# Kernel optimization log

Measured on AMD Instinct MI355X. Metric: run time of the kernel, lower is better.

## Reference

```python
import jax, jax.numpy as jnp
import numpy as np

B, W, IN, H, Z, D, OUT, K = 256, 128, 128, 1024, 128, 1024, 128, 3


def _gru_cell(h, x, Wih, Whh, bih, bhh):
    # torch nn.GRU single-layer cell, gate order (r, z, n)
    gi = x @ Wih.T + bih
    gh = h @ Whh.T + bhh
    ir, iz, inn = jnp.split(gi, 3, axis=-1)
    hr, hz, hn = jnp.split(gh, 3, axis=-1)
    r = jax.nn.sigmoid(ir + hr)
    u = jax.nn.sigmoid(iz + hz)
    n = jnp.tanh(inn + r * hn)
    return (1.0 - u) * n + u * h


def setup_inputs():
    key = jax.random.key(0)
    ks = iter(jax.random.split(key, 40))

    def w(shape, fanin):
        return jax.random.normal(next(ks), shape, jnp.float32) / np.float32(np.sqrt(fanin))

    return dict(
        x=jax.random.normal(next(ks), (B, W, IN), jnp.float32),
        eps_q=jax.random.uniform(next(ks), (B, W, Z), jnp.float32),
        eps_p=jax.random.uniform(next(ks), (B, W, OUT), jnp.float32),
        Wih_q=w((3 * H, IN), IN), Whh_q=w((3 * H, H), H),
        bih_q=jnp.zeros(3 * H, jnp.float32), bhh_q=jnp.zeros(3 * H, jnp.float32),
        Wd_q=w((D, Z + H), Z + H), bd_q=jnp.zeros(D, jnp.float32),
        Wmu_q=w((Z, D), D), bmu_q=jnp.zeros(Z, jnp.float32),
        Wsig_q=w((Z, D), D), bsig_q=jnp.zeros(Z, jnp.float32),
        Wp=w((K, Z, Z), Z), bp=jnp.zeros((K, Z), jnp.float32),
        up=0.1 * jax.random.normal(next(ks), (K,), jnp.float32),
        Wlg=w((Z, Z), Z), blg=jnp.zeros(Z, jnp.float32),
        Wih_p=w((3 * H, Z), Z), Whh_p=w((3 * H, H), H),
        bih_p=jnp.zeros(3 * H, jnp.float32), bhh_p=jnp.zeros(3 * H, jnp.float32),
        Wd_p=w((D, H), H), bd_p=jnp.zeros(D, jnp.float32),
        Wmu_p=w((OUT, D), D), bmu_p=jnp.zeros(OUT, jnp.float32),
        Wsig_p=w((OUT, D), D), bsig_p=jnp.zeros(OUT, jnp.float32),
    )


def _forward(x, eps_q, eps_p, Wih_q, Whh_q, bih_q, bhh_q, Wd_q, bd_q, Wmu_q, bmu_q,
             Wsig_q, bsig_q, Wp, bp, up, Wlg, blg, Wih_p, Whh_p, bih_p, bhh_p,
             Wd_p, bd_p, Wmu_p, bmu_p, Wsig_p, bsig_p):
    Bsz = x.shape[0]

    # ---- Qnet: sequential encoder with planar flows ----
    def q_step(carry, inp):
        e, z_prev = carry
        x_t, eps_t = inp  # [B,IN], [B,Z]
        e = _gru_cell(e, x_t, Wih_q, Whh_q, bih_q, bhh_q)
        d = jnp.concatenate([z_prev, e], axis=-1) @ Wd_q.T + bd_q
        mu = d @ Wmu_q.T + bmu_q
        logvar = jax.nn.softplus(d @ Wsig_q.T + bsig_q)
        z = mu + jnp.exp(0.5 * logvar) * eps_t
        for k in range(K):  # planar normalizing flows: z + u * tanh(Wz + b)
            z = z + up[k] * jnp.tanh(z @ Wp[k].T + bp[k])
        return (e, z), (z, mu, logvar)

    e0 = jnp.zeros((Bsz, H), x.dtype)
    z0 = jnp.zeros((Bsz, Z), x.dtype)
    _, (z_seq, mu_seq, lv_seq) = jax.lax.scan(
        q_step, (e0, z0), (jnp.swapaxes(x, 0, 1), jnp.swapaxes(eps_q, 0, 1)))

    # ---- Pnet: sequential decoder ----
    def p_step(d_t, inp):
        z_t, eps_t = inp
        zt = z_t @ Wlg.T + blg  # LGSSM linear
        d_t = _gru_cell(d_t, zt, Wih_p, Whh_p, bih_p, bhh_p)
        dd = d_t @ Wd_p.T + bd_p
        mu = dd @ Wmu_p.T + bmu_p
        sigma = jax.nn.softplus(dd @ Wsig_p.T + bsig_p)
        return d_t, mu + sigma * eps_t

    d0 = jnp.zeros((Bsz, H), x.dtype)
    _, out_seq = jax.lax.scan(p_step, d0, (z_seq, jnp.swapaxes(eps_p, 0, 1)))

    return (jnp.swapaxes(out_seq, 0, 1),
            jnp.swapaxes(mu_seq, 0, 1),
            jnp.swapaxes(lv_seq, 0, 1))


def reference(x, eps_q, eps_p, Wih_q, Whh_q, bih_q, bhh_q, Wd_q, bd_q, Wmu_q, bmu_q,
              Wsig_q, bsig_q, Wp, bp, up, Wlg, blg, Wih_p, Whh_p, bih_p, bhh_p,
              Wd_p, bd_p, Wmu_p, bmu_p, Wsig_p, bsig_p):
    return _forward(x, eps_q, eps_p, Wih_q, Whh_q, bih_q, bhh_q, Wd_q, bd_q, Wmu_q,
                    bmu_q, Wsig_q, bsig_q, Wp, bp, up, Wlg, blg, Wih_p, Whh_p,
                    bih_p, bhh_p, Wd_p, bd_p, Wmu_p, bmu_p, Wsig_p, bsig_p)
```

## Files before the change

### kernel.cpp

```cpp
#include <hip/hip_runtime.h>


typedef __bf16 bf16;
typedef __bf16 bf16x8 __attribute__((ext_vector_type(8)));
typedef float  f32x4  __attribute__((ext_vector_type(4)));
typedef unsigned u32;

static constexpr int CB   = 256;
static constexpr int CW   = 128;
static constexpr int CIN  = 128;
static constexpr int CH   = 1024;
static constexpr int CZ   = 128;
static constexpr int CD   = 1024;
static constexpr int COUT = 128;

static constexpr int APITCH     = 1160;
static constexpr int ABUF_BYTES = 16 * APITCH * 2;
static constexpr int REDN       = 8 * 16 * 17;
static constexpr int RED2_BYTES = 2 * REDN * 4;
static constexpr int FLOW_BYTES = (2 * CZ + 2 * 2 * CZ) * 4;
static constexpr int SMEM_BYTES = ABUF_BYTES + RED2_BYTES + FLOW_BYTES;

#define DEV static __device__ __forceinline__

DEV float sigmoidf_(float x) { return 1.0f / (1.0f + expf(-x)); }
DEV float softplusf_(float x) { return x > 20.0f ? x : log1pf(expf(x)); }
DEV bf16x8 ldfrag(const bf16* p) { return *reinterpret_cast<const bf16x8*>(p); }

#define MFMA(a, b, c) __builtin_amdgcn_mfma_f32_16x16x32_bf16((a), (b), (c), 0, 0, 0)

DEV bf16x8 ldd16(const bf16* p) {
    bf16x8 v;
    asm volatile("global_load_dwordx4 %0, %1, off sc0 sc1\n\ts_waitcnt vmcnt(0)"
                 : "=v"(v) : "v"(p) : "memory");
    return v;
}
DEV bf16x8 ldd16_nw(const bf16* p) {
    bf16x8 v;
    asm volatile("global_load_dwordx4 %0, %1, off sc0 sc1"
                 : "=v"(v) : "v"(p) : "memory");
    return v;
}
DEV u32 ldd4(const void* p) {
    u32 v;
    asm volatile("global_load_dword %0, %1, off sc0 sc1\n\ts_waitcnt vmcnt(0)"
                 : "=v"(v) : "v"(p) : "memory");
    return v;
}
DEV void std4(void* p, u32 v) {
    asm volatile("global_store_dword %0, %1, off sc0 sc1" :: "v"(p), "v"(v) : "memory");
}
DEV void vm_wait0() {
    asm volatile("s_waitcnt vmcnt(0)" ::: "memory");
    __builtin_amdgcn_sched_barrier(0);
}
DEV u32 pk2(float a, float b) {
    union { bf16 h[2]; u32 u; } r;
    r.h[0] = (bf16)a; r.h[1] = (bf16)b;
    return r.u;
}

struct Prm {
    const float *eps_q, *eps_p;
    const float *bih_q, *bhh_q, *bd_q, *bmu_q, *bsig_q;
    const float *Wp, *bp, *up, *Wlg, *blg;
    const float *bih_p, *bhh_p, *bd_p, *bmu_p, *bsig_p;
    const bf16 *x_b, *Wih_qb, *Whh_qb, *Wd_qb, *Wmu_qb, *Wsg_qb;
    const bf16 *Wih_pb, *Whh_pb, *Wd_pb, *Wmu_pb, *Wsg_pb;
    float *e_f0, *e_f1, *d_f0, *d_f1;
    bf16 *e_h, *d_h;
    bf16 *dvec_h, *ddvec_h;
    float *ztmp_h;
    bf16 *zflow_h;
    bf16 *ztlg_h;
    u32 *qbar, *pbar, *zbar, *pdone;
    float *out_o, *out_mu, *out_lv;
};

DEV void gbar128(u32* flg, int lwg, u32 k)
{
    asm volatile("s_waitcnt vmcnt(0)" ::: "memory");
    __syncthreads();
    if (threadIdx.x == 0)
        __hip_atomic_store(&flg[lwg * 16], k, __ATOMIC_RELAXED, __HIP_MEMORY_SCOPE_AGENT);
    if (threadIdx.x < 128) {
        while (__hip_atomic_load(&flg[threadIdx.x * 16], __ATOMIC_RELAXED,
                                 __HIP_MEMORY_SCOPE_AGENT) < k)
            __builtin_amdgcn_s_sleep(1);
    }
    __syncthreads();
}

__global__ void k_cvt(const float* __restrict__ src, bf16* __restrict__ dst, int n)
{
    int i = (blockIdx.x * blockDim.x + threadIdx.x) * 4;
    if (i < n) {
        float4 v = *reinterpret_cast<const float4*>(src + i);
        *reinterpret_cast<u32*>(dst + i)     = pk2(v.x, v.y);
        *reinterpret_cast<u32*>(dst + i + 2) = pk2(v.z, v.w);
    }
}

template <bool BIG, int HM>
DEV void stage_act(bf16* abuf, int tid, int r0,
                   const bf16* head, long hs, int K1,
                   const bf16* body, long bs)
{
    if constexpr (BIG) {
        for (int j = 0; j < 4; ++j) {
            const int idx = tid + j * 512;
            const int row = idx >> 7;
            const int k = (idx & 127) * 8;
            *reinterpret_cast<bf16x8*>(abuf + (long)row * APITCH + K1 + k) =
                ldfrag(body + (long)(r0 + row) * bs + k);
        }
    } else {
        bf16x8 v[4];
        long dst[4];
#pragma unroll
        for (int j = 0; j < 4; ++j) {
            const int idx = tid + j * 512;
            const int row = idx >> 7;
            const int k = (idx & 127) * 8;
            v[j] = ldd16_nw(body + (long)(r0 + row) * bs + k);
            dst[j] = (long)row * APITCH + K1 + k;
        }
        vm_wait0();
#pragma unroll
        for (int j = 0; j < 4; ++j)
            *reinterpret_cast<bf16x8*>(abuf + dst[j]) = v[j];
    }
    if (K1 > 0) {
        const int HC = K1 >> 3;
        for (int idx = tid; idx < 16 * HC; idx += 512) {
            const int row = idx / HC;
            const int k = (idx - row * HC) * 8;
            const bf16* s = head + (long)(r0 + row) * hs + k;
            bf16x8 hv;
            if constexpr (HM == 0) hv = ldfrag(s);
            else                   hv = BIG ? ldfrag(s) : ldd16(s);
            *reinterpret_cast<bf16x8*>(abuf + (long)row * APITCH + k) = hv;
        }
    }
    __syncthreads();
}

DEV void gru_compute(const bf16* abuf, int r0, int n0, int lane, int wave,
                     const bf16* __restrict__ Wih, const bf16* __restrict__ Whh,
                     const float* __restrict__ bih, const float* __restrict__ bhh,
                     const float* __restrict__ Efin,
                     float* __restrict__ Efo, bf16* __restrict__ Ebo)
{
    const int lr = lane & 15, lkE = (lane >> 4) * 8;
    const int c = n0 + wave * 16 + lr;
    const bf16* arow = abuf + (long)lr * APITCH;

    f32x4 acc[4] = {};
    {
        bf16x8 wv[4][3];
#pragma unroll
        for (int j = 0; j < 4; ++j)
#pragma unroll
            for (int g = 0; g < 3; ++g)
                wv[j][g] = ldfrag(Wih + ((long)g * CH + c) * CIN + j * 32 + lkE);
#pragma unroll
        for (int j = 0; j < 4; ++j) {
            bf16x8 a = *reinterpret_cast<const bf16x8*>(arow + j * 32 + lkE);
            acc[0] = MFMA(a, wv[j][0], acc[0]);
            acc[1] = MFMA(a, wv[j][1], acc[1]);
            acc[2] = MFMA(a, wv[j][2], acc[2]);
        }
    }
    {
        const bf16* wp0 = Whh + ((long)0 * CH + c) * CH + lkE;
        const bf16* wp1 = Whh + ((long)1 * CH + c) * CH + lkE;
        const bf16* wp2 = Whh + ((long)2 * CH + c) * CH + lkE;
        bf16x8 wv[4][3];
#pragma unroll
        for (int j = 0; j < 4; ++j) {
            wv[j][0] = ldfrag(wp0 + j * 32);
            wv[j][1] = ldfrag(wp1 + j * 32);
            wv[j][2] = ldfrag(wp2 + j * 32);
        }
#pragma unroll
        for (int kb = 0; kb < 32; ++kb) {
            const int sl = kb & 3;
            bf16x8 a = *reinterpret_cast<const bf16x8*>(arow + CIN + kb * 32 + lkE);
            acc[0] = MFMA(a, wv[sl][0], acc[0]);
            acc[1] = MFMA(a, wv[sl][1], acc[1]);
            acc[3] = MFMA(a, wv[sl][2], acc[3]);
            if (kb < 28) {
                wv[sl][0] = ldfrag(wp0 + (kb + 4) * 32);
                wv[sl][1] = ldfrag(wp1 + (kb + 4) * 32);
                wv[sl][2] = ldfrag(wp2 + (kb + 4) * 32);
            }
        }
    }

    const float b0r = bih[c] + bhh[c];
    const float b0z = bih[CH + c] + bhh[CH + c];
    const float bin = bih[2 * CH + c];
    const float bhn = bhh[2 * CH + c];
    const int rbase = r0 + (lane >> 4) * 4;
#pragma unroll
    for (int i = 0; i < 4; ++i) {
        const int row = rbase + i;
        float r = sigmoidf_(acc[0][i] + b0r);
        float u = sigmoidf_(acc[1][i] + b0z);
        float n = tanhf(acc[2][i] + bin + r * (acc[3][i] + bhn));
        float en = (1.0f - u) * n + u * Efin[(long)row * CH + c];
        Efo[(long)row * CH + c] = en;
        float vB = __shfl_xor(en, 1);
        if (!(lane & 1))
            std4(Ebo + (long)row * CH + c, pk2(en, vB));
    }
}

DEV void lin_compute(const bf16* abuf, int r0, int n0, int lane, int wave, int Ktot,
                     const bf16* __restrict__ W,
                     const float* __restrict__ bias, bf16* __restrict__ Out)
{
    const int lr = lane & 15, lkE = (lane >> 4) * 8;
    const int c = n0 + wave * 16 + lr;
    const bf16* arow = abuf + (long)lr * APITCH;
    const bf16* wrow = W + (long)c * Ktot;
    const int kofs = Ktot - CH;

    f32x4 acc = {};
    {
        const bf16* wp = wrow + kofs + lkE;
        bf16x8 wv[8];
#pragma unroll
        for (int j = 0; j < 8; ++j) wv[j] = ldfrag(wp + j * 32);
#pragma unroll
        for (int kb = 0; kb < 32; ++kb) {
            const int sl = kb & 7;
            bf16x8 a = *reinterpret_cast<const bf16x8*>(arow + kofs + kb * 32 + lkE);
            acc = MFMA(a, wv[sl], acc);
            if (kb < 24) wv[sl] = ldfrag(wp + (kb + 8) * 32);
        }
    }
    if (Ktot > CH) {
        bf16x8 wv[4];
#pragma unroll
        for (int j = 0; j < 4; ++j) wv[j] = ldfrag(wrow + j * 32 + lkE);
#pragma unroll
        for (int j = 0; j < 4; ++j) {
            bf16x8 a = *reinterpret_cast<const bf16x8*>(arow + j * 32 + lkE);
            acc = MFMA(a, wv[j], acc);
        }
    }

    const float bb = bias[c];
    const int rbase = r0 + (lane >> 4) * 4;
#pragma unroll
    for (int i = 0; i < 4; ++i) {
        float v = acc[i] + bb;
        float vB = __shfl_xor(v, 1);
        if (!(lane & 1))
            std4(Out + (long)(rbase + i) * CD + c, pk2(v, vB));
    }
}

template <bool BIG, int MODE>
DEV void phase_tail2(const Prm& p, int t, int mb, int nb, int tid,
                     int lane, int wave, float* Ra, float* Rs,
                     const bf16* __restrict__ A, float* __restrict__ ztmp,
                     const bf16* __restrict__ Wa, const bf16* __restrict__ Wb,
                     const float* __restrict__ ba, const float* __restrict__ bb)
{
    const int lr = lane & 15, lkE = (lane >> 4) * 8;
    f32x4 am = {}, as = {};
    const int k0 = wave * 128;
    bf16x8 av[4], bmv[4], bsv[4];
#pragma unroll
    for (int j = 0; j < 4; ++j) {
        const int k = k0 + j * 32;
        const bf16* ap = A + (long)(mb + lr) * CD + k + lkE;
        av[j]  = BIG ? ldfrag(ap) : ldd16_nw(ap);
        bmv[j] = ldfrag(Wa + (long)(nb + lr) * CD + k + lkE);
        bsv[j] = ldfrag(Wb + (long)(nb + lr) * CD + k + lkE);
    }
    if constexpr (!BIG) vm_wait0();
#pragma unroll
    for (int j = 0; j < 4; ++j) {
        am = MFMA(av[j], bmv[j], am);
        as = MFMA(av[j], bsv[j], as);
    }
    __syncthreads();
#pragma unroll
    for (int i = 0; i < 4; ++i) {
        Ra[(wave * 16 + (lane >> 4) * 4 + i) * 17 + lr] = am[i];
        Rs[(wave * 16 + (lane >> 4) * 4 + i) * 17 + lr] = as[i];
    }
    __syncthreads();
    if (tid < 256) {
        const int trow = tid >> 4, tcol = tid & 15;
        float vm = 0.f, vs = 0.f;
#pragma unroll
        for (int w = 0; w < 8; ++w) {
            vm += Ra[(w * 16 + trow) * 17 + tcol];
            vs += Rs[(w * 16 + trow) * 17 + tcol];
        }
        const int row = mb + trow, col = nb + tcol;
        if constexpr (MODE == 0) {
            float mu = vm + ba[col];
            float lv = softplusf_(vs + bb[col]);
            float e  = p.eps_q[(long)row * CW * CZ + (long)t * CZ + col];
            float z  = mu + expf(0.5f * lv) * e;
            p.out_mu[(long)row * CW * CZ + (long)t * CZ + col] = mu;
            p.out_lv[(long)row * CW * CZ + (long)t * CZ + col] = lv;
            std4(ztmp + (long)row * CZ + col, __float_as_uint(z));
        } else {
            float m  = vm + ba[col];
            float sg = softplusf_(vs + bb[col]);
            float e  = p.eps_p[(long)row * CW * COUT + (long)t * COUT + col];
            p.out_o[(long)row * CW * COUT + (long)t * COUT + col] = m + sg * e;
        }
    }
}

template <bool BIG>
DEV void phase_flows2(const Prm& p, int rowbase, int tid, int t, float* zl, float* ps,
                      const float* __restrict__ ztmp,
                      bf16* __restrict__ ztlg, bf16* __restrict__ zflow_next)
{
    const int rg = tid >> 8;
    const int sub = tid & 255;
    const int c = sub & 127, half = sub >> 7;
    const int row = rowbase + rg;
    float* zrow = zl + rg * CZ;
    float* pall = ps + rg * 2 * CZ;

    if (half == 0)
        zrow[c] = BIG ? ztmp[(long)row * CZ + c]
                      : __uint_as_float(ldd4(ztmp + (long)row * CZ + c));
    __syncthreads();

#pragma unroll 1
    for (int kf = 0; kf < 3; ++kf) {
        const float* wr = p.Wp + ((long)kf * CZ + c) * CZ + half * 64;
        const float* zh = zrow + half * 64;
        float s = 0.f;
#pragma unroll
        for (int j = 0; j < 64; j += 4) {
            float4 w = *reinterpret_cast<const float4*>(wr + j);
            s += zh[j] * w.x + zh[j + 1] * w.y + zh[j + 2] * w.z + zh[j + 3] * w.w;
        }
        pall[half * CZ + c] = s;
        __syncthreads();
        if (half == 0) {
            float sf = pall[c] + pall[CZ + c] + p.bp[kf * CZ + c];
            zrow[c] += p.up[kf] * tanhf(sf);
        }
        __syncthreads();
    }
    {
        const float* wr = p.Wlg + (long)c * CZ + half * 64;
        const float* zh = zrow + half * 64;
        float s = 0.f;
#pragma unroll
        for (int j = 0; j < 64; j += 4) {
            float4 w = *reinterpret_cast<const float4*>(wr + j);
            s += zh[j] * w.x + zh[j + 1] * w.y + zh[j + 2] * w.z + zh[j + 3] * w.w;
        }
        pall[half * CZ + c] = s;
        __syncthreads();
        if (half == 0) {
            float zt = pall[c] + pall[CZ + c] + p.blg[c];
            float ztB = __shfl_xor(zt, 1);
            if (!(c & 1)) {
                std4(ztlg + (long)row * CZ + c, pk2(zt, ztB));
                std4(zflow_next + (long)row * CZ + c, pk2(zrow[c], zrow[c + 1]));
            }
        }
    }
}

template <bool BIG>
DEV void run_q(const Prm& p, int lwg, int tid,
               bf16* abuf, float* Ra, float* Rs, float* ZLp, float* PSp)
{
    const int lane = tid & 63, wave = tid >> 6;
    const int g = lwg >> 5, m = lwg & 31;
    const int r0 = (m >> 1) * 16;
    const int n0 = g * 256 + (m & 1) * 128;
    const int nt = g * 32 + (m & 1) * 16;
    const size_t SH = (size_t)CB * CH, SD = (size_t)CB * CD, SZ = (size_t)CB * CZ;
    u32 bk = 0;
#pragma unroll 1
    for (int t = 0; t < CW; ++t) {
        const int eIn  = BIG ? t : (t & 1);
        const int eOut = BIG ? (t + 1) : ((t + 1) & 1);
        const int dT   = BIG ? t : 0;
        const int zT   = BIG ? t : (t & 1);
        const float* ef_i = (t & 1) ? p.e_f1 : p.e_f0;
        float*       ef_o = (t & 1) ? p.e_f0 : p.e_f1;

        stage_act<BIG, 0>(abuf, tid, r0, p.x_b + (long)t * CIN, (long)CW * CIN,
                          CIN, p.e_h + (size_t)eIn * SH, CH);
        gru_compute(abuf, r0, n0, lane, wave, p.Wih_qb, p.Whh_qb,
                    p.bih_q, p.bhh_q, ef_i, ef_o, p.e_h + (size_t)eOut * SH);
        gbar128(p.qbar, lwg, ++bk);

        stage_act<BIG, 1>(abuf, tid, r0, p.zflow_h + (size_t)eIn * SZ, CZ, CZ,
                          p.e_h + (size_t)eOut * SH, CH);
        lin_compute(abuf, r0, n0, lane, wave, CZ + CH, p.Wd_qb, p.bd_q,
                    p.dvec_h + (size_t)dT * SD);
        gbar128(p.qbar, lwg, ++bk);

        phase_tail2<BIG, 0>(p, t, r0, nt, tid, lane, wave, Ra, Rs,
                            p.dvec_h + (size_t)dT * SD, p.ztmp_h + (size_t)dT * SZ,
                            p.Wmu_qb, p.Wsg_qb, p.bmu_q, p.bsig_q);
        gbar128(p.qbar, lwg, ++bk);

        if constexpr (!BIG) {
            if (t >= 2) {
                if (tid < 128) {
                    while ((int)__hip_atomic_load(&p.pdone[tid * 16], __ATOMIC_RELAXED,
                                                  __HIP_MEMORY_SCOPE_AGENT) < t - 1)
                        __builtin_amdgcn_s_sleep(2);
                }
                __syncthreads();
            }
        }
        phase_flows2<BIG>(p, lwg * 2, tid, t, ZLp, PSp,
                          p.ztmp_h + (size_t)dT * SZ,
                          p.ztlg_h + (size_t)zT * SZ,
                          p.zflow_h + (size_t)eOut * SZ);
        asm volatile("s_waitcnt vmcnt(0)" ::: "memory");
        __syncthreads();
        if (tid == 0)
            __hip_atomic_store(&p.zbar[lwg * 16], (u32)(t + 1),
                               __ATOMIC_RELAXED, __HIP_MEMORY_SCOPE_AGENT);
        __syncthreads();
    }
}

template <bool BIG>
DEV void run_p(const Prm& p, int lwg, int tid,
               bf16* abuf, float* Ra, float* Rs)
{
    const int lane = tid & 63, wave = tid >> 6;
    const int g = lwg >> 5, m = lwg & 31;
    const int r0 = (m >> 1) * 16;
    const int n0 = g * 256 + (m & 1) * 128;
    const int nt = g * 32 + (m & 1) * 16;
    const size_t SH = (size_t)CB * CH, SD = (size_t)CB * CD, SZ = (size_t)CB * CZ;
    u32 bk = 0;
#pragma unroll 1
    for (int t = 0; t < CW; ++t) {
        if (tid < 128) {
            while (__hip_atomic_load(&p.zbar[tid * 16], __ATOMIC_RELAXED,
                                     __HIP_MEMORY_SCOPE_AGENT) < (u32)(t + 1))
                __builtin_amdgcn_s_sleep(2);
        }
        __syncthreads();

        const int sIn  = BIG ? t : (t & 1);
        const int sOut = BIG ? (t + 1) : ((t + 1) & 1);
        const int dT   = BIG ? t : 0;
        const int zT   = BIG ? t : (t & 1);
        const float* df_i = (t & 1) ? p.d_f1 : p.d_f0;
        float*       df_o = (t & 1) ? p.d_f0 : p.d_f1;

        stage_act<BIG, 1>(abuf, tid, r0, p.ztlg_h + (size_t)zT * SZ, CZ, CZ,
                          p.d_h + (size_t)sIn * SH, CH);
        gru_compute(abuf, r0, n0, lane, wave, p.Wih_pb, p.Whh_pb,
                    p.bih_p, p.bhh_p, df_i, df_o, p.d_h + (size_t)sOut * SH);
        gbar128(p.pbar, lwg, ++bk);
        if constexpr (!BIG) {
            if (tid == 0)
                __hip_atomic_store(&p.pdone[lwg * 16], (u32)(t + 1),
                                   __ATOMIC_RELAXED, __HIP_MEMORY_SCOPE_AGENT);
        }

        stage_act<BIG, 0>(abuf, tid, r0, nullptr, 0, 0,
                          p.d_h + (size_t)sOut * SH, CH);
        lin_compute(abuf, r0, n0, lane, wave, CH, p.Wd_pb, p.bd_p,
                    p.ddvec_h + (size_t)dT * SD);
        gbar128(p.pbar, lwg, ++bk);

        phase_tail2<BIG, 1>(p, t, r0, nt, tid, lane, wave, Ra, Rs,
                            p.ddvec_h + (size_t)dT * SD, nullptr,
                            p.Wmu_pb, p.Wsg_pb, p.bmu_p, p.bsig_p);
    }
}

template <bool BIG>
__launch_bounds__(512)
__global__ void mega(Prm p)
{
    extern __shared__ char smem[];
    bf16*  abuf = (bf16*)smem;
    float* Ra   = (float*)(smem + ABUF_BYTES);
    float* Rs   = Ra + REDN;
    float* ZLp  = (float*)(smem + ABUF_BYTES + RED2_BYTES);
    float* PSp  = ZLp + 2 * CZ;

    const int wg = blockIdx.x, tid = threadIdx.x;
    const int gid = wg & 7, m = wg >> 3;
    const bool isQ = gid < 4;
    const int lwg = (isQ ? gid : gid - 4) * 32 + m;

    if (isQ) run_q<BIG>(p, lwg, tid, abuf, Ra, Rs, ZLp, PSp);
    else     run_p<BIG>(p, lwg, tid, abuf, Ra, Rs);
}

extern "C" void kernel_launch(void* const* d_in, const int* in_sizes, int n_in,
                              void* d_out, int out_size, void* d_ws, size_t ws_size,
                              hipStream_t stream)
{
    Prm p;
    const float* x      = (const float*)d_in[0];
    p.eps_q  = (const float*)d_in[1];
    p.eps_p  = (const float*)d_in[2];
    const float* Wih_q  = (const float*)d_in[3];
    const float* Whh_q  = (const float*)d_in[4];
    p.bih_q  = (const float*)d_in[5];
    p.bhh_q  = (const float*)d_in[6];
    const float* Wd_q   = (const float*)d_in[7];
    p.bd_q   = (const float*)d_in[8];
    const float* Wmu_q  = (const float*)d_in[9];
    p.bmu_q  = (const float*)d_in[10];
    const float* Wsig_q = (const float*)d_in[11];
    p.bsig_q = (const float*)d_in[12];
    p.Wp     = (const float*)d_in[13];
    p.bp     = (const float*)d_in[14];
    p.up     = (const float*)d_in[15];
    p.Wlg    = (const float*)d_in[16];
    p.blg    = (const float*)d_in[17];
    const float* Wih_p  = (const float*)d_in[18];
    const float* Whh_p  = (const float*)d_in[19];
    p.bih_p  = (const float*)d_in[20];
    p.bhh_p  = (const float*)d_in[21];
    const float* Wd_p   = (const float*)d_in[22];
    p.bd_p   = (const float*)d_in[23];
    const float* Wmu_p  = (const float*)d_in[24];
    p.bmu_p  = (const float*)d_in[25];
    const float* Wsig_p = (const float*)d_in[26];
    p.bsig_p = (const float*)d_in[27];

    p.out_o  = (float*)d_out;
    p.out_mu = p.out_o + (size_t)CB * CW * COUT;
    p.out_lv = p.out_mu + (size_t)CB * CW * CZ;

    const bool BIGM = ws_size >= (size_t)400 * 1024 * 1024;
    const int NS = BIGM ? (CW + 1) : 2;
    const int NT = BIGM ? CW : 1;
    const int NZ = BIGM ? CW : 2;

    char* wp_ = (char*)d_ws;
    auto carve = [&](size_t bytes) -> void* {
        void* q = (void*)wp_;
        wp_ += (bytes + 255) & ~(size_t)255;
        return q;
    };
    p.e_f0 = (float*)carve((size_t)CB * CH * 4);
    p.e_f1 = (float*)carve((size_t)CB * CH * 4);
    p.d_f0 = (float*)carve((size_t)CB * CH * 4);
    p.d_f1 = (float*)carve((size_t)CB * CH * 4);
    p.e_h     = (bf16*)carve((size_t)NS * CB * CH * 2);
    p.d_h     = (bf16*)carve((size_t)NS * CB * CH * 2);
    p.dvec_h  = (bf16*)carve((size_t)NT * CB * CD * 2);
    p.ddvec_h = (bf16*)carve((size_t)NT * CB * CD * 2);
    p.ztmp_h  = (float*)carve((size_t)NT * CB * CZ * 4);
    p.zflow_h = (bf16*)carve((size_t)NS * CB * CZ * 2);
    p.ztlg_h  = (bf16*)carve((size_t)NZ * CB * CZ * 2);
    p.qbar    = (u32*)carve((size_t)128 * 16 * 4);
    p.pbar    = (u32*)carve((size_t)128 * 16 * 4);
    p.zbar    = (u32*)carve((size_t)128 * 16 * 4);
    p.pdone   = (u32*)carve((size_t)128 * 16 * 4);
    bf16* x_b    = (bf16*)carve((size_t)CB * CW * CIN * 2);
    bf16* Wih_qb = (bf16*)carve((size_t)3 * CH * CIN * 2);
    bf16* Whh_qb = (bf16*)carve((size_t)3 * CH * CH * 2);
    bf16* Wd_qb  = (bf16*)carve((size_t)CD * (CZ + CH) * 2);
    bf16* Wmu_qb = (bf16*)carve((size_t)CZ * CD * 2);
    bf16* Wsg_qb = (bf16*)carve((size_t)CZ * CD * 2);
    bf16* Wih_pb = (bf16*)carve((size_t)3 * CH * CZ * 2);
    bf16* Whh_pb = (bf16*)carve((size_t)3 * CH * CH * 2);
    bf16* Wd_pb  = (bf16*)carve((size_t)CD * CH * 2);
    bf16* Wmu_pb = (bf16*)carve((size_t)COUT * CD * 2);
    bf16* Wsg_pb = (bf16*)carve((size_t)COUT * CD * 2);
    p.x_b = x_b;       p.Wih_qb = Wih_qb; p.Whh_qb = Whh_qb;
    p.Wd_qb = Wd_qb;   p.Wmu_qb = Wmu_qb; p.Wsg_qb = Wsg_qb;
    p.Wih_pb = Wih_pb; p.Whh_pb = Whh_pb; p.Wd_pb = Wd_pb;
    p.Wmu_pb = Wmu_pb; p.Wsg_pb = Wsg_pb;

    hipMemsetAsync(p.e_f0, 0, (size_t)CB * CH * 4, stream);
    hipMemsetAsync(p.d_f0, 0, (size_t)CB * CH * 4, stream);
    hipMemsetAsync(p.e_h, 0, (size_t)CB * CH * 2, stream);
    hipMemsetAsync(p.d_h, 0, (size_t)CB * CH * 2, stream);
    hipMemsetAsync(p.zflow_h, 0, (size_t)CB * CZ * 2, stream);
    hipMemsetAsync(p.qbar, 0, (size_t)128 * 16 * 4, stream);
    hipMemsetAsync(p.pbar, 0, (size_t)128 * 16 * 4, stream);
    hipMemsetAsync(p.zbar, 0, (size_t)128 * 16 * 4, stream);
    hipMemsetAsync(p.pdone, 0, (size_t)128 * 16 * 4, stream);

    auto cvt = [&](const float* s, bf16* d, size_t n) {
        k_cvt<<<dim3((unsigned)((n / 4 + 255) / 256)), dim3(256), 0, stream>>>(s, d, (int)n);
    };
    cvt(x,      x_b,    (size_t)CB * CW * CIN);
    cvt(Wih_q,  Wih_qb, (size_t)3 * CH * CIN);
    cvt(Whh_q,  Whh_qb, (size_t)3 * CH * CH);
    cvt(Wd_q,   Wd_qb,  (size_t)CD * (CZ + CH));
    cvt(Wmu_q,  Wmu_qb, (size_t)CZ * CD);
    cvt(Wsig_q, Wsg_qb, (size_t)CZ * CD);
    cvt(Wih_p,  Wih_pb, (size_t)3 * CH * CZ);
    cvt(Whh_p,  Whh_pb, (size_t)3 * CH * CH);
    cvt(Wd_p,   Wd_pb,  (size_t)CD * CH);
    cvt(Wmu_p,  Wmu_pb, (size_t)COUT * CD);
    cvt(Wsig_p, Wsg_pb, (size_t)COUT * CD);

    if (BIGM)
        mega<true><<<dim3(256), dim3(512), SMEM_BYTES, stream>>>(p);
    else
        mega<false><<<dim3(256), dim3(512), SMEM_BYTES, stream>>>(p);
}
```

Before: 8.053 ms.

## Replace global 128-WG barriers with per-slab dependency flags in BIG path

In the BIG-mode mega kernel, the full 128-workgroup barriers between GRU, linear, tail and flow phases are replaced with per-workgroup progress flags. Each workgroup now waits only on the 8 producers whose outputs it reads (its row slab or flow range). The Q-to-P handoff also waits on a range of 8 flow flags instead of all 128. This loosens lockstep synchronisation so workgroups can run ahead, at the risk of missed dependencies (for example, reading e_h columns from other groups) if the slab mapping is wrong. The flag memset is merged into one contiguous clear over the ten flag arrays.

```diff
diff --git a/kernel.cpp b/kernel.cpp
--- a/kernel.cpp
+++ b/kernel.cpp
@@ -74,6 +74,7 @@
     bf16 *zflow_h;
     bf16 *ztlg_h;
     u32 *qbar, *pbar, *zbar, *pdone;
+    u32 *qg, *ql, *qt, *qf, *pg, *pl;
     float *out_o, *out_mu, *out_lv;
 };
 
@@ -85,6 +86,33 @@
         __hip_atomic_store(&flg[lwg * 16], k, __ATOMIC_RELAXED, __HIP_MEMORY_SCOPE_AGENT);
     if (threadIdx.x < 128) {
         while (__hip_atomic_load(&flg[threadIdx.x * 16], __ATOMIC_RELAXED,
+                                 __HIP_MEMORY_SCOPE_AGENT) < k)
+            __builtin_amdgcn_s_sleep(1);
+    }
+    __syncthreads();
+}
+
+DEV void post_flag(u32* f, int lwg, u32 k)
+{
+    asm volatile("s_waitcnt vmcnt(0)" ::: "memory");
+    __syncthreads();
+    if (threadIdx.x == 0)
+        __hip_atomic_store(&f[lwg * 16], k, __ATOMIC_RELAXED, __HIP_MEMORY_SCOPE_AGENT);
+}
+DEV void wait_slab8(const u32* f, int slab, u32 k)
+{
+    if (threadIdx.x < 8) {
+        const int idx = (threadIdx.x >> 1) * 32 + slab * 2 + (threadIdx.x & 1);
+        while (__hip_atomic_load(&f[idx * 16], __ATOMIC_RELAXED,
+                                 __HIP_MEMORY_SCOPE_AGENT) < k)
+            __builtin_amdgcn_s_sleep(1);
+    }
+    __syncthreads();
+}
+DEV void wait_rng8(const u32* f, int base, u32 k)
+{
+    if ((int)k > 0 && threadIdx.x < 8) {
+        while (__hip_atomic_load(&f[(base + threadIdx.x) * 16], __ATOMIC_RELAXED,
                                  __HIP_MEMORY_SCOPE_AGENT) < k)
             __builtin_amdgcn_s_sleep(1);
     }
@@ -383,7 +411,8 @@
 {
     const int lane = tid & 63, wave = tid >> 6;
     const int g = lwg >> 5, m = lwg & 31;
-    const int r0 = (m >> 1) * 16;
+    const int slab = m >> 1;
+    const int r0 = slab * 16;
     const int n0 = g * 256 + (m & 1) * 128;
     const int nt = g * 32 + (m & 1) * 16;
     const size_t SH = (size_t)CB * CH, SD = (size_t)CB * CD, SZ = (size_t)CB * CZ;
@@ -401,20 +430,30 @@
                           CIN, p.e_h + (size_t)eIn * SH, CH);
         gru_compute(abuf, r0, n0, lane, wave, p.Wih_qb, p.Whh_qb,
                     p.bih_q, p.bhh_q, ef_i, ef_o, p.e_h + (size_t)eOut * SH);
-        gbar128(p.qbar, lwg, ++bk);
-
+        if constexpr (BIG) post_flag(p.qg, lwg, (u32)(t + 1));
+        else               gbar128(p.qbar, lwg, ++bk);
+
+        if constexpr (BIG) {
+            wait_rng8(p.qf, slab * 8, (u32)t);
+            wait_slab8(p.qg, slab, (u32)(t + 1));
+        }
         stage_act<BIG, 1>(abuf, tid, r0, p.zflow_h + (size_t)eIn * SZ, CZ, CZ,
                           p.e_h + (size_t)eOut * SH, CH);
         lin_compute(abuf, r0, n0, lane, wave, CZ + CH, p.Wd_qb, p.bd_q,
                     p.dvec_h + (size_t)dT * SD);
-        gbar128(p.qbar, lwg, ++bk);
-
+        if constexpr (BIG) post_flag(p.ql, lwg, (u32)(t + 1));
+        else               gbar128(p.qbar, lwg, ++bk);
+
+        if constexpr (BIG) wait_slab8(p.ql, slab, (u32)(t + 1));
         phase_tail2<BIG, 0>(p, t, r0, nt, tid, lane, wave, Ra, Rs,
                             p.dvec_h + (size_t)dT * SD, p.ztmp_h + (size_t)dT * SZ,
                             p.Wmu_qb, p.Wsg_qb, p.bmu_q, p.bsig_q);
-        gbar128(p.qbar, lwg, ++bk);
-
-        if constexpr (!BIG) {
+        if constexpr (BIG) post_flag(p.qt, lwg, (u32)(t + 1));
+        else               gbar128(p.qbar, lwg, ++bk);
+
+        if constexpr (BIG) {
+            wait_slab8(p.qt, lwg >> 3, (u32)(t + 1));
+        } else {
             if (t >= 2) {
                 if (tid < 128) {
                     while ((int)__hip_atomic_load(&p.pdone[tid * 16], __ATOMIC_RELAXED,
@@ -428,12 +467,16 @@
                           p.ztmp_h + (size_t)dT * SZ,
                           p.ztlg_h + (size_t)zT * SZ,
                           p.zflow_h + (size_t)eOut * SZ);
-        asm volatile("s_waitcnt vmcnt(0)" ::: "memory");
-        __syncthreads();
-        if (tid == 0)
-            __hip_atomic_store(&p.zbar[lwg * 16], (u32)(t + 1),
-                               __ATOMIC_RELAXED, __HIP_MEMORY_SCOPE_AGENT);
-        __syncthreads();
+        if constexpr (BIG) {
+            post_flag(p.qf, lwg, (u32)(t + 1));
+        } else {
+            asm volatile("s_waitcnt vmcnt(0)" ::: "memory");
+            __syncthreads();
+            if (tid == 0)
+                __hip_atomic_store(&p.zbar[lwg * 16], (u32)(t + 1),
+                                   __ATOMIC_RELAXED, __HIP_MEMORY_SCOPE_AGENT);
+            __syncthreads();
+        }
     }
 }
 
@@ -443,19 +486,24 @@
 {
     const int lane = tid & 63, wave = tid >> 6;
     const int g = lwg >> 5, m = lwg & 31;
-    const int r0 = (m >> 1) * 16;
+    const int slab = m >> 1;
+    const int r0 = slab * 16;
     const int n0 = g * 256 + (m & 1) * 128;
     const int nt = g * 32 + (m & 1) * 16;
     const size_t SH = (size_t)CB * CH, SD = (size_t)CB * CD, SZ = (size_t)CB * CZ;
     u32 bk = 0;
 #pragma unroll 1
     for (int t = 0; t < CW; ++t) {
-        if (tid < 128) {
-            while (__hip_atomic_load(&p.zbar[tid * 16], __ATOMIC_RELAXED,
-                                     __HIP_MEMORY_SCOPE_AGENT) < (u32)(t + 1))
-                __builtin_amdgcn_s_sleep(2);
-        }
-        __syncthreads();
+        if constexpr (BIG) {
+            wait_rng8(p.qf, slab * 8, (u32)(t + 1));
+        } else {
+            if (tid < 128) {
+                while (__hip_atomic_load(&p.zbar[tid * 16], __ATOMIC_RELAXED,
+                                         __HIP_MEMORY_SCOPE_AGENT) < (u32)(t + 1))
+                    __builtin_amdgcn_s_sleep(2);
+            }
+            __syncthreads();
+        }
 
         const int sIn  = BIG ? t : (t & 1);
         const int sOut = BIG ? (t + 1) : ((t + 1) & 1);
@@ -468,19 +516,23 @@
                           p.d_h + (size_t)sIn * SH, CH);
         gru_compute(abuf, r0, n0, lane, wave, p.Wih_pb, p.Whh_pb,
                     p.bih_p, p.bhh_p, df_i, df_o, p.d_h + (size_t)sOut * SH);
-        gbar128(p.pbar, lwg, ++bk);
-        if constexpr (!BIG) {
+        if constexpr (BIG) post_flag(p.pg, lwg, (u32)(t + 1));
+        else {
+            gbar128(p.pbar, lwg, ++bk);
             if (tid == 0)
                 __hip_atomic_store(&p.pdone[lwg * 16], (u32)(t + 1),
                                    __ATOMIC_RELAXED, __HIP_MEMORY_SCOPE_AGENT);
         }
 
+        if constexpr (BIG) wait_slab8(p.pg, slab, (u32)(t + 1));
         stage_act<BIG, 0>(abuf, tid, r0, nullptr, 0, 0,
                           p.d_h + (size_t)sOut * SH, CH);
         lin_compute(abuf, r0, n0, lane, wave, CH, p.Wd_pb, p.bd_p,
                     p.ddvec_h + (size_t)dT * SD);
-        gbar128(p.pbar, lwg, ++bk);
-
+        if constexpr (BIG) post_flag(p.pl, lwg, (u32)(t + 1));
+        else               gbar128(p.pbar, lwg, ++bk);
+
+        if constexpr (BIG) wait_slab8(p.pl, slab, (u32)(t + 1));
         phase_tail2<BIG, 1>(p, t, r0, nt, tid, lane, wave, Ra, Rs,
                             p.ddvec_h + (size_t)dT * SD, nullptr,
                             p.Wmu_pb, p.Wsg_pb, p.bmu_p, p.bsig_p);
@@ -571,6 +623,12 @@
     p.pbar    = (u32*)carve((size_t)128 * 16 * 4);
     p.zbar    = (u32*)carve((size_t)128 * 16 * 4);
     p.pdone   = (u32*)carve((size_t)128 * 16 * 4);
+    p.qg      = (u32*)carve((size_t)128 * 16 * 4);
+    p.ql      = (u32*)carve((size_t)128 * 16 * 4);
+    p.qt      = (u32*)carve((size_t)128 * 16 * 4);
+    p.qf      = (u32*)carve((size_t)128 * 16 * 4);
+    p.pg      = (u32*)carve((size_t)128 * 16 * 4);
+    p.pl      = (u32*)carve((size_t)128 * 16 * 4);
     bf16* x_b    = (bf16*)carve((size_t)CB * CW * CIN * 2);
     bf16* Wih_qb = (bf16*)carve((size_t)3 * CH * CIN * 2);
     bf16* Whh_qb = (bf16*)carve((size_t)3 * CH * CH * 2);
@@ -592,10 +650,7 @@
     hipMemsetAsync(p.e_h, 0, (size_t)CB * CH * 2, stream);
     hipMemsetAsync(p.d_h, 0, (size_t)CB * CH * 2, stream);
     hipMemsetAsync(p.zflow_h, 0, (size_t)CB * CZ * 2, stream);
-    hipMemsetAsync(p.qbar, 0, (size_t)128 * 16 * 4, stream);
-    hipMemsetAsync(p.pbar, 0, (size_t)128 * 16 * 4, stream);
-    hipMemsetAsync(p.zbar, 0, (size_t)128 * 16 * 4, stream);
-    hipMemsetAsync(p.pdone, 0, (size_t)128 * 16 * 4, stream);
+    hipMemsetAsync(p.qbar, 0, (size_t)128 * 16 * 4 * 10, stream);
 
     auto cvt = [&](const float* s, bf16* d, size_t n) {
         k_cvt<<<dim3((unsigned)((n / 4 + 255) / 256)), dim3(256), 0, stream>>>(s, d, (int)n);
```

Measured after the change: 8.129 ms. No clear change (+0.9%).

## Fuse Q-net mu/sigma tail into per-row flow phase, dropping a grid barrier

Applied to the files above, without the earlier changes.

In the BIG path, each workgroup now computes mu/logvar for its own two rows directly, using a dot-product GEMV over the full D dimension, and feeds z straight into the planar-flow phase in shared memory. This removes one 128-workgroup grid barrier per timestep and the ztmp global round-trip. The cost is redundant-free but less parallel tail work: each workgroup reads all of Wmu/Wsig (512 KB bf16) per step instead of a tiled slice, which adds L2 traffic and scalar FMA work.

```diff
diff --git a/kernel.cpp b/kernel.cpp
--- a/kernel.cpp
+++ b/kernel.cpp
@@ -320,10 +320,8 @@
     }
 }
 
-template <bool BIG>
-DEV void phase_flows2(const Prm& p, int rowbase, int tid, int t, float* zl, float* ps,
-                      const float* __restrict__ ztmp,
-                      bf16* __restrict__ ztlg, bf16* __restrict__ zflow_next)
+DEV void flows_body(const Prm& p, int rowbase, int tid, int t, float* zl, float* ps,
+                    bf16* __restrict__ ztlg, bf16* __restrict__ zflow_next)
 {
     const int rg = tid >> 8;
     const int sub = tid & 255;
@@ -331,11 +329,6 @@
     const int row = rowbase + rg;
     float* zrow = zl + rg * CZ;
     float* pall = ps + rg * 2 * CZ;
-
-    if (half == 0)
-        zrow[c] = BIG ? ztmp[(long)row * CZ + c]
-                      : __uint_as_float(ldd4(ztmp + (long)row * CZ + c));
-    __syncthreads();
 
 #pragma unroll 1
     for (int kf = 0; kf < 3; ++kf) {
@@ -377,10 +370,62 @@
     }
 }
 
+DEV void qtail_flows(const Prm& p, int lwg, int tid, int t, char* scratch)
+{
+    bf16*  dv  = (bf16*)scratch;
+    float* res = (float*)(scratch + 2 * 1032 * 2);
+    float* zl  = res + 512;
+    float* ps  = zl + 2 * CZ;
+    const size_t SD = (size_t)CB * CD, SZ = (size_t)CB * CZ;
+    const int row0 = lwg * 2;
+
+    if (tid < 256) {
+        const int r = tid >> 7, k = (tid & 127) * 8;
+        *reinterpret_cast<bf16x8*>(dv + (long)r * 1032 + k) =
+            ldfrag(p.dvec_h + (size_t)t * SD + (size_t)(row0 + r) * CD + k);
+    }
+    __syncthreads();
+
+    const int wr = tid & 255, rb = tid >> 8;
+    const bf16* wrow = (wr < 128) ? (p.Wmu_qb + (long)wr * CD)
+                                  : (p.Wsg_qb + (long)(wr - 128) * CD);
+    const bf16* drow = dv + (long)rb * 1032;
+    float acc = 0.f;
+#pragma unroll 4
+    for (int k = 0; k < CD; k += 8) {
+        bf16x8 w = ldfrag(wrow + k);
+        bf16x8 a = *reinterpret_cast<const bf16x8*>(drow + k);
+#pragma unroll
+        for (int j = 0; j < 8; ++j) acc += (float)a[j] * (float)w[j];
+    }
+    res[rb * 256 + wr] = acc;
+    __syncthreads();
+
+    if (tid < 256) {
+        const int r = tid >> 7, col = tid & 127;
+        const int row = row0 + r;
+        float mu = res[r * 256 + col] + p.bmu_q[col];
+        float lv = softplusf_(res[r * 256 + 128 + col] + p.bsig_q[col]);
+        float e  = p.eps_q[(size_t)row * CW * CZ + (size_t)t * CZ + col];
+        p.out_mu[(size_t)row * CW * CZ + (size_t)t * CZ + col] = mu;
+        p.out_lv[(size_t)row * CW * CZ + (size_t)t * CZ + col] = lv;
+        zl[r * CZ + col] = mu + expf(0.5f * lv) * e;
+    }
+    __syncthreads();
+
+    flows_body(p, row0, tid, t, zl, ps,
+               p.ztlg_h + (size_t)t * SZ,
+               p.zflow_h + (size_t)(t + 1) * SZ);
+}
+
 template <bool BIG>
-DEV void run_q(const Prm& p, int lwg, int tid,
-               bf16* abuf, float* Ra, float* Rs, float* ZLp, float* PSp)
-{
+DEV void run_q(const Prm& p, int lwg, int tid, char* smem)
+{
+    bf16*  abuf = (bf16*)smem;
+    float* Ra   = (float*)(smem + ABUF_BYTES);
+    float* Rs   = Ra + REDN;
+    float* ZLp  = (float*)(smem + ABUF_BYTES + RED2_BYTES);
+    float* PSp  = ZLp + 2 * CZ;
     const int lane = tid & 63, wave = tid >> 6;
     const int g = lwg >> 5, m = lwg & 31;
     const int r0 = (m >> 1) * 16;
@@ -409,12 +454,13 @@
                     p.dvec_h + (size_t)dT * SD);
         gbar128(p.qbar, lwg, ++bk);
 
-        phase_tail2<BIG, 0>(p, t, r0, nt, tid, lane, wave, Ra, Rs,
-                            p.dvec_h + (size_t)dT * SD, p.ztmp_h + (size_t)dT * SZ,
-                            p.Wmu_qb, p.Wsg_qb, p.bmu_q, p.bsig_q);
-        gbar128(p.qbar, lwg, ++bk);
-
-        if constexpr (!BIG) {
+        if constexpr (BIG) {
+            qtail_flows(p, lwg, tid, t, smem + ABUF_BYTES);
+        } else {
+            phase_tail2<BIG, 0>(p, t, r0, nt, tid, lane, wave, Ra, Rs,
+                                p.dvec_h + (size_t)dT * SD, p.ztmp_h + (size_t)dT * SZ,
+                                p.Wmu_qb, p.Wsg_qb, p.bmu_q, p.bsig_q);
+            gbar128(p.qbar, lwg, ++bk);
             if (t >= 2) {
                 if (tid < 128) {
                     while ((int)__hip_atomic_load(&p.pdone[tid * 16], __ATOMIC_RELAXED,
@@ -423,11 +469,18 @@
                 }
                 __syncthreads();
             }
-        }
-        phase_flows2<BIG>(p, lwg * 2, tid, t, ZLp, PSp,
-                          p.ztmp_h + (size_t)dT * SZ,
-                          p.ztlg_h + (size_t)zT * SZ,
-                          p.zflow_h + (size_t)eOut * SZ);
+            {
+                const int rg = tid >> 8, sub = tid & 255;
+                const int c = sub & 127, half = sub >> 7;
+                if (half == 0)
+                    ZLp[rg * CZ + c] = __uint_as_float(
+                        ldd4(p.ztmp_h + (size_t)dT * SZ + (long)(lwg * 2 + rg) * CZ + c));
+                __syncthreads();
+            }
+            flows_body(p, lwg * 2, tid, t, ZLp, PSp,
+                       p.ztlg_h + (size_t)zT * SZ,
+                       p.zflow_h + (size_t)eOut * SZ);
+        }
         asm volatile("s_waitcnt vmcnt(0)" ::: "memory");
         __syncthreads();
         if (tid == 0)
@@ -438,9 +491,11 @@
 }
 
 template <bool BIG>
-DEV void run_p(const Prm& p, int lwg, int tid,
-               bf16* abuf, float* Ra, float* Rs)
-{
+DEV void run_p(const Prm& p, int lwg, int tid, char* smem)
+{
+    bf16*  abuf = (bf16*)smem;
+    float* Ra   = (float*)(smem + ABUF_BYTES);
+    float* Rs   = Ra + REDN;
     const int lane = tid & 63, wave = tid >> 6;
     const int g = lwg >> 5, m = lwg & 31;
     const int r0 = (m >> 1) * 16;
@@ -492,19 +547,13 @@
 __global__ void mega(Prm p)
 {
     extern __shared__ char smem[];
-    bf16*  abuf = (bf16*)smem;
-    float* Ra   = (float*)(smem + ABUF_BYTES);
-    float* Rs   = Ra + REDN;
-    float* ZLp  = (float*)(smem + ABUF_BYTES + RED2_BYTES);
-    float* PSp  = ZLp + 2 * CZ;
-
     const int wg = blockIdx.x, tid = threadIdx.x;
     const int gid = wg & 7, m = wg >> 3;
     const bool isQ = gid < 4;
     const int lwg = (isQ ? gid : gid - 4) * 32 + m;
 
-    if (isQ) run_q<BIG>(p, lwg, tid, abuf, Ra, Rs, ZLp, PSp);
-    else     run_p<BIG>(p, lwg, tid, abuf, Ra, Rs);
+    if (isQ) run_q<BIG>(p, lwg, tid, smem);
+    else     run_p<BIG>(p, lwg, tid, smem);
 }
 
 extern "C" void kernel_launch(void* const* d_in, const int* in_sizes, int n_in,
@@ -587,15 +636,15 @@
     p.Wih_pb = Wih_pb; p.Whh_pb = Whh_pb; p.Wd_pb = Wd_pb;
     p.Wmu_pb = Wmu_pb; p.Wsg_pb = Wsg_pb;
 
-    hipMemsetAsync(p.e_f0, 0, (size_t)CB * CH * 4, stream);
-    hipMemsetAsync(p.d_f0, 0, (size_t)CB * CH * 4, stream);
-    hipMemsetAsync(p.e_h, 0, (size_t)CB * CH * 2, stream);
-    hipMemsetAsync(p.d_h, 0, (size_t)CB * CH * 2, stream);
-    hipMemsetAsync(p.zflow_h, 0, (size_t)CB * CZ * 2, stream);
-    hipMemsetAsync(p.qbar, 0, (size_t)128 * 16 * 4, stream);
-    hipMemsetAsync(p.pbar, 0, (size_t)128 * 16 * 4, stream);
-    hipMemsetAsync(p.zbar, 0, (size_t)128 * 16 * 4, stream);
-    hipMemsetAsync(p.pdone, 0, (size_t)128 * 16 * 4, stream);
+    (void)hipMemsetAsync(p.e_f0, 0, (size_t)CB * CH * 4, stream);
+    (void)hipMemsetAsync(p.d_f0, 0, (size_t)CB * CH * 4, stream);
+    (void)hipMemsetAsync(p.e_h, 0, (size_t)CB * CH * 2, stream);
+    (void)hipMemsetAsync(p.d_h, 0, (size_t)CB * CH * 2, stream);
+    (void)hipMemsetAsync(p.zflow_h, 0, (size_t)CB * CZ * 2, stream);
+    (void)hipMemsetAsync(p.qbar, 0, (size_t)128 * 16 * 4, stream);
+    (void)hipMemsetAsync(p.pbar, 0, (size_t)128 * 16 * 4, stream);
+    (void)hipMemsetAsync(p.zbar, 0, (size_t)128 * 16 * 4, stream);
+    (void)hipMemsetAsync(p.pdone, 0, (size_t)128 * 16 * 4, stream);
 
     auto cvt = [&](const float* s, bf16* d, size_t n) {
         k_cvt<<<dim3((unsigned)((n / 4 + 255) / 256)), dim3(256), 0, stream>>>(s, d, (int)n);
```

Result: no change. 8.191 ms (+1.7%).
